# Kernel tuning notes

Measured on AMD Instinct MI355X. Metric: run time of the kernel, lower is better.

Reference implementation:

```python
import jax, jax.numpy as jnp
import numpy as np

N = 50000      # nodes
E = 800000     # edges (avg degree 16)
NFEAT = 256
NHID = 128
NCLASS = 40
NLAYERS_MID = 13  # gc2..gc14


def setup_inputs() -> dict:
    key = jax.random.key(0)
    ks = jax.random.split(key, 16)
    stdv_h = 1.0 / np.sqrt(NHID)     # GraphConvolution stdv = 1/sqrt(out_features)
    stdv_c = 1.0 / np.sqrt(NCLASS)
    u = lambda k, shape, s: jax.random.uniform(k, shape, jnp.float32, -s, s)
    return {
        "x": jax.random.normal(ks[0], (N, NFEAT), jnp.float32),
        "edge_src": jax.random.randint(ks[1], (E,), 0, N, jnp.int32),
        "edge_dst": jax.random.randint(ks[2], (E,), 0, N, jnp.int32),
        "edge_weight": jax.random.uniform(ks[3], (E,), jnp.float32),
        # skip-branch linear (self.weight / self.bias)
        "W0": u(ks[4], (NFEAT, NHID), stdv_h),
        "b0": u(ks[5], (NHID,), stdv_h),
        # gc1: nfeat -> nhid
        "W1": u(ks[6], (NFEAT, NHID), stdv_h),
        "b1": u(ks[7], (NHID,), stdv_h),
        # gc2..gc14: nhid -> nhid, stacked
        "Wmid": u(ks[8], (NLAYERS_MID, NHID, NHID), stdv_h),
        "bmid": u(ks[9], (NLAYERS_MID, NHID), stdv_h),
        # gc15: 14*nhid -> nclass
        "W15": u(ks[10], (14 * NHID, NCLASS), stdv_c),
        "b15": u(ks[11], (NCLASS,), stdv_c),
    }


def reference(x, edge_src, edge_dst, edge_weight, W0, b0, W1, b1, Wmid, bmid, W15, b15):
    n = x.shape[0]

    def gcn(h, W, b):
        # support = h @ W ; out = spmm(adj, support) + b  (adj as weighted edge list)
        support = h @ W
        msgs = support[edge_src] * edge_weight[:, None]           # [E, d]
        agg = jax.ops.segment_sum(msgs, edge_dst, num_segments=n)  # [N, d]
        return agg + b

    z = x @ W0 + b0
    x1 = jax.nn.relu(gcn(x, W1, b1)) + z

    def step(h, Wb):
        W, b = Wb
        hn = jax.nn.relu(gcn(h, W, b)) + h
        return hn, hn

    _, xs = jax.lax.scan(step, x1, (Wmid, bmid))   # xs: [13, N, NHID] = x2..x14
    all_x = jnp.concatenate([x1[None], xs], axis=0)  # [14, N, NHID] = x1..x14
    # concat order in torch code: (x14, x13, ..., x1)
    x_cat = jnp.swapaxes(all_x[::-1], 0, 1).reshape(n, 14 * NHID)
    # dropout is identity in eval mode
    x15 = gcn(x_cat, W15, b15)
    return jax.nn.log_softmax(x15, axis=1)
```

## Files before the change

### kernel.cpp

```cpp
#include <hip/hip_runtime.h>
#include <stdint.h>

#define NN 50000
#define EE 800000
#define DH 128
#define NC 40
#define KCAT (14*DH)
#define CAP 64

typedef __bf16 bf16x8 __attribute__((ext_vector_type(8)));
typedef float floatx4 __attribute__((ext_vector_type(4)));

#define GLOAD_LDS16(gp, lp)                                                          \
  __builtin_amdgcn_global_load_lds(                                                  \
      (const __attribute__((address_space(1))) uint32_t*)(gp),                       \
      (__attribute__((address_space(3))) uint32_t*)(lp), 16, 0, 0)

__device__ __forceinline__ float bf2f(unsigned short u) {
  union { uint32_t i; float f; } v; v.i = ((uint32_t)u) << 16; return v.f;
}
__device__ __forceinline__ unsigned short f2bf(float f) {
  union { float f; uint32_t i; } v; v.f = f;
  uint32_t x = v.i;
  uint32_t r = (x + 0x7fffu + ((x >> 16) & 1u)) >> 16;
  return (unsigned short)r;
}

__global__ void init_counts_detect(int* counts, const unsigned short* xw) {
  int i = blockIdx.x * blockDim.x + threadIdx.x;
  if (i < NN) counts[i] = 0;
  if (blockIdx.x == 0) {
    int t = threadIdx.x;
    int wild = 0;
    for (int k = t; k < 4096; k += 256) {
      unsigned e = (xw[k] >> 7) & 0xFF;
      if (e >= 0x90) wild++;
    }
    __shared__ int red[256];
    red[t] = wild;
    __syncthreads();
    for (int s = 128; s > 0; s >>= 1) {
      if (t < s) red[t] += red[t + s];
      __syncthreads();
    }
    if (t == 0) counts[NN] = red[0];
  }
}

__global__ void convert_f4(const void* in, unsigned short* outp, int n4, const int* flag) {
  bool isf32 = (*flag) > 32;
  for (int i = blockIdx.x * blockDim.x + threadIdx.x; i < n4;
       i += gridDim.x * blockDim.x) {
    ushort4 o;
    if (isf32) {
      float4 v = ((const float4*)in)[i];
      o.x = f2bf(v.x); o.y = f2bf(v.y); o.z = f2bf(v.z); o.w = f2bf(v.w);
    } else {
      o = ((const ushort4*)in)[i];
    }
    ((ushort4*)outp)[i] = o;
  }
}

__global__ void convert_bias(const void* b0, const void* b1, const void* bm,
                             const void* b15, unsigned short* bb, const int* flag) {
  bool isf32 = (*flag) > 32;
  int i = blockIdx.x * blockDim.x + threadIdx.x;
  if (i >= 1960) return;
  const void* src; int off;
  if (i < 128)        { src = b0;  off = i; }
  else if (i < 256)   { src = b1;  off = i - 128; }
  else if (i < 1920)  { src = bm;  off = i - 256; }
  else                { src = b15; off = i - 1920; }
  bb[i] = isf32 ? f2bf(((const float*)src)[off]) : ((const unsigned short*)src)[off];
}

__global__ void transpose_w(const void* B, unsigned short* BT,
                            int L, int K, int M, int Mpad, const int* flag) {
  bool isf32 = (*flag) > 32;
  int total = L * Mpad * K;
  for (int idx = blockIdx.x * blockDim.x + threadIdx.x; idx < total;
       idx += gridDim.x * blockDim.x) {
    int k = idx % K;
    int n = (idx / K) % Mpad;
    int l = idx / (K * Mpad);
    unsigned short v = 0;
    if (n < M) {
      size_t si = (size_t)l * K * M + (size_t)k * M + n;
      v = isf32 ? f2bf(((const float*)B)[si]) : ((const unsigned short*)B)[si];
    }
    BT[idx] = v;
  }
}

__global__ void build_ell(const int* __restrict__ src, const int* __restrict__ dst,
                          const void* __restrict__ w,
                          int* __restrict__ cnt, int2* __restrict__ ell,
                          const int* __restrict__ flag) {
  bool isf32 = (*flag) > 32;
  int e = blockIdx.x * blockDim.x + threadIdx.x;
  if (e >= EE) return;
  int d = dst[e];
  if ((unsigned)d >= NN) return;
  int p = atomicAdd(&cnt[d], 1);
  if (p >= CAP) return;
  int s = src[e];
  float wf = isf32 ? ((const float*)w)[e] : bf2f(((const unsigned short*)w)[e]);
  if ((unsigned)s >= NN) { s = 0; wf = 0.f; }
  union { float f; int i; } wv; wv.f = wf;
  ell[(size_t)d * CAP + p] = make_int2(s, wv.i);
}

__global__ void pad_ell(const int* __restrict__ cnt, int2* __restrict__ ell) {
  int wave = threadIdx.x >> 6, lane = threadIdx.x & 63;
  int row = blockIdx.x * 4 + wave;
  if (row >= NN) return;
  int n = cnt[row];
  if (n > CAP) n = CAP;
  int padn = (n + 7) & ~7;
  if (lane >= n && lane < padn) ell[(size_t)row * CAP + lane] = make_int2(0, 0);
}

__global__ __launch_bounds__(256) void gemm_first(
    const unsigned short* __restrict__ A,
    const unsigned short* __restrict__ BT,
    unsigned short* __restrict__ C0,
    unsigned short* __restrict__ C1,
    const unsigned short* __restrict__ bias) {
  __shared__ unsigned short As[64 * 256];
  int t = threadIdx.x;
  int wave = t >> 6, lane = t & 63;
  int q = lane >> 4, mn = lane & 15;
  int r0 = blockIdx.x * 64;

  #pragma unroll
  for (int cc = 0; cc < 8; ++cc) {
    int L = cc * 4096 + t * 16;
    int row = L >> 9;
    int colb = (L & 511) ^ ((row & 7) << 4);
    int gr = r0 + row; if (gr >= NN) gr = NN - 1;
    GLOAD_LDS16((const char*)A + (size_t)gr * 512 + colb, (char*)As + L);
  }
  __syncthreads();

  floatx4 acc[4][4];
  floatx4 zf = {0.f, 0.f, 0.f, 0.f};
  #pragma unroll
  for (int i = 0; i < 4; ++i)
    #pragma unroll
    for (int j = 0; j < 4; ++j) acc[i][j] = zf;

  #pragma unroll
  for (int ks = 0; ks < 8; ++ks) {
    bf16x8 fa[4], fb[4];
    #pragma unroll
    for (int i = 0; i < 4; ++i) {
      int row = i * 16 + mn;
      fa[i] = *(const bf16x8*)((const char*)As + row * 512 +
                               ((ks * 64 + q * 16) ^ ((row & 7) << 4)));
    }
    #pragma unroll
    for (int j = 0; j < 4; ++j)
      fb[j] = *(const bf16x8*)((const char*)BT +
                               (size_t)(wave * 64 + j * 16 + mn) * 512 + ks * 64 + q * 16);
    #pragma unroll
    for (int i = 0; i < 4; ++i)
      #pragma unroll
      for (int j = 0; j < 4; ++j)
        acc[i][j] = __builtin_amdgcn_mfma_f32_16x16x32_bf16(fa[i], fb[j], acc[i][j], 0, 0, 0);
  }

  #pragma unroll
  for (int j = 0; j < 4; ++j) {
    int col = wave * 64 + j * 16 + mn;
    bool is0 = col < 128;
    int ccol = is0 ? col : col - 128;
    unsigned short* Cp = is0 ? C0 : C1;
    float badd = is0 ? bf2f(bias[ccol]) : 0.f;
    #pragma unroll
    for (int i = 0; i < 4; ++i) {
      int rbase = r0 + i * 16 + q * 4;
      #pragma unroll
      for (int rr = 0; rr < 4; ++rr) {
        int row = rbase + rr;
        if (row < NN) Cp[(size_t)row * 128 + ccol] = f2bf(acc[i][j][rr] + badd);
      }
    }
  }
}

__global__ __launch_bounds__(256) void gemm_mid(
    const unsigned short* __restrict__ A,
    const unsigned short* __restrict__ BT,
    unsigned short* __restrict__ C) {
  __shared__ unsigned short As[32 * 128];
  int t = threadIdx.x;
  int wave = t >> 6, lane = t & 63;
  int q = lane >> 4, mn = lane & 15;
  int r0 = blockIdx.x * 32;

  #pragma unroll
  for (int cc = 0; cc < 2; ++cc) {
    int L = cc * 4096 + t * 16;
    int row = L >> 8;
    int colb = (L & 255) ^ ((row & 7) << 4);
    int gr = r0 + row; if (gr >= NN) gr = NN - 1;
    GLOAD_LDS16((const char*)A + (size_t)gr * (KCAT * 2) + colb, (char*)As + L);
  }
  __syncthreads();

  floatx4 acc[2][2];
  floatx4 zf = {0.f, 0.f, 0.f, 0.f};
  #pragma unroll
  for (int i = 0; i < 2; ++i)
    #pragma unroll
    for (int j = 0; j < 2; ++j) acc[i][j] = zf;

  #pragma unroll
  for (int ks = 0; ks < 4; ++ks) {
    bf16x8 fa[2], fb[2];
    #pragma unroll
    for (int i = 0; i < 2; ++i) {
      int row = i * 16 + mn;
      fa[i] = *(const bf16x8*)((const char*)As + row * 256 +
                               ((ks * 64 + q * 16) ^ ((row & 7) << 4)));
    }
    #pragma unroll
    for (int j = 0; j < 2; ++j)
      fb[j] = *(const bf16x8*)((const char*)BT +
                               (size_t)(wave * 32 + j * 16 + mn) * 256 + ks * 64 + q * 16);
    #pragma unroll
    for (int i = 0; i < 2; ++i)
      #pragma unroll
      for (int j = 0; j < 2; ++j)
        acc[i][j] = __builtin_amdgcn_mfma_f32_16x16x32_bf16(fa[i], fb[j], acc[i][j], 0, 0, 0);
  }

  #pragma unroll
  for (int i = 0; i < 2; ++i) {
    int rbase = r0 + i * 16 + q * 4;
    #pragma unroll
    for (int j = 0; j < 2; ++j) {
      int col = wave * 32 + j * 16 + mn;
      #pragma unroll
      for (int rr = 0; rr < 4; ++rr) {
        int row = rbase + rr;
        if (row < NN) C[(size_t)row * 128 + col] = f2bf(acc[i][j][rr]);
      }
    }
  }
}

__global__ __launch_bounds__(256) void gemm_cat3(
    const unsigned short* __restrict__ A,
    const unsigned short* __restrict__ BT,
    float* __restrict__ C) {
  __shared__ unsigned short As[2][64 * 128];
  int t = threadIdx.x;
  int wave = t >> 6, lane = t & 63;
  int q = lane >> 4, mn = lane & 15;
  int r0 = blockIdx.x * 64;

  floatx4 acc[3];
  floatx4 zf = {0.f, 0.f, 0.f, 0.f};
  #pragma unroll
  for (int j = 0; j < 3; ++j) acc[j] = zf;

  const char* bbase[3];
  #pragma unroll
  for (int j = 0; j < 3; ++j)
    bbase[j] = (const char*)BT + (size_t)(j * 16 + mn) * 3584 + q * 16;

  auto stage = [&](int c) {
    #pragma unroll
    for (int cc = 0; cc < 4; ++cc) {
      int L = cc * 4096 + t * 16;
      int row = L >> 8;
      int colb = (L & 255) ^ ((row & 7) << 4);
      int gr = r0 + row; if (gr >= NN) gr = NN - 1;
      GLOAD_LDS16((const char*)A + (size_t)gr * 3584 + c * 256 + colb,
                  (char*)As[c & 1] + L);
    }
  };

  stage(0);
  __syncthreads();
  int rloc = wave * 16 + mn;
  int rsw = (rloc & 7) << 4;
  for (int c = 0; c < 14; ++c) {
    bf16x8 fb[3][4];
    #pragma unroll
    for (int ks = 0; ks < 4; ++ks)
      #pragma unroll
      for (int j = 0; j < 3; ++j)
        fb[j][ks] = *(const bf16x8*)(bbase[j] + c * 256 + ks * 64);
    asm volatile("" ::: "memory");
    if (c + 1 < 14) stage(c + 1);
    asm volatile("" ::: "memory");
    const char* buf = (const char*)As[c & 1];
    #pragma unroll
    for (int ks = 0; ks < 4; ++ks) {
      bf16x8 fa = *(const bf16x8*)(buf + rloc * 256 + ((ks * 64 + q * 16) ^ rsw));
      #pragma unroll
      for (int j = 0; j < 3; ++j)
        acc[j] = __builtin_amdgcn_mfma_f32_16x16x32_bf16(fa, fb[j][ks], acc[j], 0, 0, 0);
    }
    if (c + 1 < 14) __syncthreads();
  }

  #pragma unroll
  for (int j = 0; j < 3; ++j) {
    int col = j * 16 + mn;
    if (col < NC) {
      #pragma unroll
      for (int rr = 0; rr < 4; ++rr) {
        int row = r0 + wave * 16 + q * 4 + rr;
        if (row < NN) C[(size_t)row * NC + col] = acc[j][rr];
      }
    }
  }
}

__global__ __launch_bounds__(256) void spmm_layer(
    const unsigned short* __restrict__ support, const int* __restrict__ cnt,
    const int2* __restrict__ ell, const unsigned short* __restrict__ bias,
    const unsigned short* __restrict__ res, int res_stride,
    unsigned short* __restrict__ out, int out_stride) {
  int wave = threadIdx.x >> 6, lane = threadIdx.x & 63;
  int row = blockIdx.x * 4 + wave;
  if (row >= NN) return;
  int n = cnt[row];
  if (n > CAP) n = CAP;
  int padn = (n + 7) & ~7;
  int2 ev = make_int2(0, 0);
  if (lane < padn) ev = ell[(size_t)row * CAP + lane];
  uint32_t bw = *(const uint32_t*)(bias + 2 * lane);
  uint32_t rw = *(const uint32_t*)(res + (size_t)row * res_stride + 2 * lane);

  float a0 = 0.f, a1 = 0.f;
  uint32_t gA[8], gB[8];
  auto load8 = [&](uint32_t* g, int j0) {
    #pragma unroll
    for (int u = 0; u < 8; ++u) {
      int s = __shfl(ev.x, j0 + u);
      g[u] = *(const uint32_t*)(support + (size_t)s * DH + 2 * lane);
    }
  };
  auto fma8 = [&](const uint32_t* g, int j0) {
    #pragma unroll
    for (int u = 0; u < 8; ++u) {
      union { int i; float f; } wv; wv.i = __shfl(ev.y, j0 + u);
      a0 += wv.f * bf2f((unsigned short)(g[u] & 0xffff));
      a1 += wv.f * bf2f((unsigned short)(g[u] >> 16));
    }
  };
  if (padn > 0) {
    load8(gA, 0);
    int b = 0;
    for (;;) {
      if (8 * (b + 1) < padn) load8(gB, 8 * (b + 1));
      fma8(gA, 8 * b);
      ++b; if (8 * b >= padn) break;
      if (8 * (b + 1) < padn) load8(gA, 8 * (b + 1));
      fma8(gB, 8 * b);
      ++b; if (8 * b >= padn) break;
    }
  }

  float v0 = fmaxf(a0 + bf2f((unsigned short)(bw & 0xffff)), 0.f) +
             bf2f((unsigned short)(rw & 0xffff));
  float v1 = fmaxf(a1 + bf2f((unsigned short)(bw >> 16)), 0.f) +
             bf2f((unsigned short)(rw >> 16));
  uint32_t o = (uint32_t)f2bf(v0) | ((uint32_t)f2bf(v1) << 16);
  *(uint32_t*)(out + (size_t)row * out_stride + 2 * lane) = o;
}

__global__ __launch_bounds__(256) void spmm_softmax_out(
    const float* __restrict__ s15, const int* __restrict__ cnt,
    const int2* __restrict__ ell, const unsigned short* __restrict__ bias,
    float* __restrict__ out) {
  int wave = threadIdx.x >> 6, lane = threadIdx.x & 63;
  int row = blockIdx.x * 4 + wave;
  if (row >= NN) return;
  int n = cnt[row];
  if (n > CAP) n = CAP;
  int padn = (n + 7) & ~7;
  int2 ev = make_int2(0, 0);
  if (lane < padn) ev = ell[(size_t)row * CAP + lane];
  int fl = lane < NC ? lane : NC - 1;
  float acc = 0.f;
  for (int j = 0; j < padn; j += 4) {
    float g[4];
    #pragma unroll
    for (int u = 0; u < 4; ++u) {
      int s = __shfl(ev.x, j + u);
      g[u] = s15[(size_t)s * NC + fl];
    }
    #pragma unroll
    for (int u = 0; u < 4; ++u) {
      union { int i; float f; } wv; wv.i = __shfl(ev.y, j + u);
      acc += wv.f * g[u];
    }
  }
  acc += bf2f(bias[fl]);
  float v = (lane < NC) ? acc : -3.0e38f;
  float m = v;
  #pragma unroll
  for (int off = 32; off > 0; off >>= 1) m = fmaxf(m, __shfl_xor(m, off));
  float e = (lane < NC) ? expf(v - m) : 0.f;
  float sum = e;
  #pragma unroll
  for (int off = 32; off > 0; off >>= 1) sum += __shfl_xor(sum, off);
  if (lane < NC) out[(size_t)row * NC + lane] = v - m - logf(sum);
}

extern "C" void kernel_launch(void* const* d_in, const int* in_sizes, int n_in,
                              void* d_out, int out_size, void* d_ws, size_t ws_size,
                              hipStream_t stream) {
  const void* x   = d_in[0];
  const int* esrc = (const int*)d_in[1];
  const int* edst = (const int*)d_in[2];
  const void* ew  = d_in[3];
  const void* W0  = d_in[4];
  const void* b0  = d_in[5];
  const void* W1  = d_in[6];
  const void* b1  = d_in[7];
  const void* Wm  = d_in[8];
  const void* bm  = d_in[9];
  const void* W15 = d_in[10];
  const void* b15 = d_in[11];
  float* out = (float*)d_out;

  char* ws = (char*)d_ws;
  size_t off = 0;
  auto alloc = [&](size_t bytes) -> void* {
    void* p = ws + off;
    off = (off + bytes + 255) & ~(size_t)255;
    return p;
  };
  unsigned short* xcat = (unsigned short*)alloc((size_t)NN * KCAT * 2);
  unsigned short* xbf  = (unsigned short*)alloc((size_t)NN * 256 * 2);
  unsigned short* supp = (unsigned short*)alloc((size_t)NN * DH * 2);
  unsigned short* zbuf = (unsigned short*)alloc((size_t)NN * DH * 2);
  float* s15           = (float*)alloc((size_t)NN * NC * 4);
  int* counts          = (int*)alloc((size_t)(NN + 1) * 4);
  int2* ell            = (int2*)alloc((size_t)NN * CAP * 8);
  unsigned short* W01T = (unsigned short*)alloc((size_t)256 * 256 * 2);
  unsigned short* WmT  = (unsigned short*)alloc((size_t)13 * 128 * 128 * 2);
  unsigned short* W15T = (unsigned short*)alloc((size_t)48 * 1792 * 2);
  unsigned short* bb   = (unsigned short*)alloc((size_t)(128 + 128 + 13 * 128 + 40) * 2);
  if (off > ws_size) return;
  int* flag = counts + NN;
  unsigned short* b0b  = bb;
  unsigned short* b1b  = bb + 128;
  unsigned short* bmb  = bb + 256;
  unsigned short* b15b = bb + 256 + 13 * 128;

  init_counts_detect<<<197, 256, 0, stream>>>(counts, (const unsigned short*)x);
  transpose_w<<<128, 256, 0, stream>>>(W0, W01T, 1, 256, 128, 128, flag);
  transpose_w<<<128, 256, 0, stream>>>(W1, W01T + 128 * 256, 1, 256, 128, 128, flag);
  transpose_w<<<832, 256, 0, stream>>>(Wm, WmT, 13, 128, 128, 128, flag);
  transpose_w<<<336, 256, 0, stream>>>(W15, W15T, 1, 1792, 40, 48, flag);
  convert_f4<<<2048, 256, 0, stream>>>(x, xbf, NN * 256 / 4, flag);
  convert_bias<<<8, 256, 0, stream>>>(b0, b1, bm, b15, bb, flag);
  build_ell<<<3125, 256, 0, stream>>>(esrc, edst, ew, counts, ell, flag);

  int gb64 = (NN + 63) / 64;
  int gb32 = (NN + 31) / 32;
  int sb   = (NN + 3) / 4;
  pad_ell<<<sb, 256, 0, stream>>>(counts, ell);
  gemm_first<<<gb64, 256, 0, stream>>>(xbf, W01T, zbuf, supp, b0b);
  spmm_layer<<<sb, 256, 0, stream>>>(supp, counts, ell, b1b, zbuf, DH,
                                     xcat + 13 * DH, KCAT);
  for (int l = 0; l < 13; ++l) {
    gemm_mid<<<gb32, 256, 0, stream>>>(xcat + (13 - l) * DH,
                                       WmT + l * 128 * 128, supp);
    spmm_layer<<<sb, 256, 0, stream>>>(supp, counts, ell, bmb + l * DH,
                                       xcat + (13 - l) * DH, KCAT,
                                       xcat + (12 - l) * DH, KCAT);
  }
  gemm_cat3<<<gb64, 256, 0, stream>>>(xcat, W15T, s15);
  spmm_softmax_out<<<sb, 256, 0, stream>>>(s15, counts, ell, b15b, out);
}
```

Before: 956.8 us.

## Slice SpMM rows across column quarters and deepen final GEMM pipeline

The SpMM layer kernel now splits each row's 128 features into four 64-byte column slices handled by separate blocks. Each wave processes four rows with 16 lanes each, so one 8-byte gather per lane becomes 16 lanes covering a contiguous 64-byte chunk. The aim is more parallelism and better memory-level concurrency for the gather-bound aggregation, at the cost of reading the ELL index data four times. The final concat GEMM moves from a 2-stage to a 4-stage LDS ring with explicit vmcnt waits and raw barriers, prefetching B fragments one step ahead, to overlap loads with MFMA work.

```diff
diff --git a/kernel.cpp b/kernel.cpp
--- a/kernel.cpp
+++ b/kernel.cpp
@@ -251,11 +251,11 @@
   }
 }
 
-__global__ __launch_bounds__(256) void gemm_cat3(
+__global__ __launch_bounds__(256) void gemm_cat4(
     const unsigned short* __restrict__ A,
     const unsigned short* __restrict__ BT,
     float* __restrict__ C) {
-  __shared__ unsigned short As[2][64 * 128];
+  __shared__ unsigned short As[4][64 * 128];
   int t = threadIdx.x;
   int wave = t >> 6, lane = t & 63;
   int q = lane >> 4, mn = lane & 15;
@@ -279,25 +279,34 @@
       int colb = (L & 255) ^ ((row & 7) << 4);
       int gr = r0 + row; if (gr >= NN) gr = NN - 1;
       GLOAD_LDS16((const char*)A + (size_t)gr * 3584 + c * 256 + colb,
-                  (char*)As[c & 1] + L);
+                  (char*)As[c & 3] + L);
     }
   };
 
+  bf16x8 fb[3][4];
+  auto loadB = [&](int c) {
+    #pragma unroll
+    for (int ks = 0; ks < 4; ++ks)
+      #pragma unroll
+      for (int j = 0; j < 3; ++j)
+        fb[j][ks] = *(const bf16x8*)(bbase[j] + c * 256 + ks * 64);
+  };
+
   stage(0);
-  __syncthreads();
+  asm volatile("" ::: "memory");
+  loadB(0);
+  asm volatile("" ::: "memory");
+  stage(1);
+  stage(2);
+
   int rloc = wave * 16 + mn;
   int rsw = (rloc & 7) << 4;
   for (int c = 0; c < 14; ++c) {
-    bf16x8 fb[3][4];
-    #pragma unroll
-    for (int ks = 0; ks < 4; ++ks)
-      #pragma unroll
-      for (int j = 0; j < 3; ++j)
-        fb[j][ks] = *(const bf16x8*)(bbase[j] + c * 256 + ks * 64);
-    asm volatile("" ::: "memory");
-    if (c + 1 < 14) stage(c + 1);
-    asm volatile("" ::: "memory");
-    const char* buf = (const char*)As[c & 1];
+    if (c == 0)      asm volatile("s_waitcnt vmcnt(8)" ::: "memory");
+    else if (c < 12) asm volatile("s_waitcnt vmcnt(4)" ::: "memory");
+    else             asm volatile("s_waitcnt vmcnt(0)" ::: "memory");
+    __builtin_amdgcn_s_barrier();
+    const char* buf = (const char*)As[c & 3];
     #pragma unroll
     for (int ks = 0; ks < 4; ++ks) {
       bf16x8 fa = *(const bf16x8*)(buf + rloc * 256 + ((ks * 64 + q * 16) ^ rsw));
@@ -305,7 +314,10 @@
       for (int j = 0; j < 3; ++j)
         acc[j] = __builtin_amdgcn_mfma_f32_16x16x32_bf16(fa, fb[j][ks], acc[j], 0, 0, 0);
     }
-    if (c + 1 < 14) __syncthreads();
+    asm volatile("" ::: "memory");
+    if (c + 1 < 14) loadB(c + 1);
+    asm volatile("" ::: "memory");
+    if (c + 3 < 14) stage(c + 3);
   }
 
   #pragma unroll
@@ -321,58 +333,72 @@
   }
 }
 
-__global__ __launch_bounds__(256) void spmm_layer(
+__global__ __launch_bounds__(256) void spmm_layer_sliced(
     const unsigned short* __restrict__ support, const int* __restrict__ cnt,
     const int2* __restrict__ ell, const unsigned short* __restrict__ bias,
     const unsigned short* __restrict__ res, int res_stride,
     unsigned short* __restrict__ out, int out_stride) {
+  int bid = blockIdx.x;
+  int slice = bid & 3;
+  int rblk = bid >> 2;
   int wave = threadIdx.x >> 6, lane = threadIdx.x & 63;
-  int row = blockIdx.x * 4 + wave;
-  if (row >= NN) return;
-  int n = cnt[row];
-  if (n > CAP) n = CAP;
+  int group = lane >> 4, gl = lane & 15;
+  int row = rblk * 16 + wave * 4 + group;
+  int colb = slice * 64 + gl * 4;
+
+  int n = cnt[row]; if (n > CAP) n = CAP;
   int padn = (n + 7) & ~7;
-  int2 ev = make_int2(0, 0);
-  if (lane < padn) ev = ell[(size_t)row * CAP + lane];
-  uint32_t bw = *(const uint32_t*)(bias + 2 * lane);
-  uint32_t rw = *(const uint32_t*)(res + (size_t)row * res_stride + 2 * lane);
-
+  const int2* erow = ell + (size_t)row * CAP;
+  int2 ev0 = (gl      < padn) ? erow[gl]      : make_int2(0, 0);
+  int2 ev1 = (gl + 16 < padn) ? erow[gl + 16] : make_int2(0, 0);
+  int2 ev2 = (gl + 32 < padn) ? erow[gl + 32] : make_int2(0, 0);
+  int2 ev3 = (gl + 48 < padn) ? erow[gl + 48] : make_int2(0, 0);
+
+  int wm = padn;
+  wm = max(wm, __shfl_xor(wm, 16));
+  wm = max(wm, __shfl_xor(wm, 32));
+
+  int srcbase = lane & 0x30;
   float a0 = 0.f, a1 = 0.f;
   uint32_t gA[8], gB[8];
-  auto load8 = [&](uint32_t* g, int j0) {
+
+  auto load8 = [&](uint32_t* g, int2 EV, int boff) {
     #pragma unroll
     for (int u = 0; u < 8; ++u) {
-      int s = __shfl(ev.x, j0 + u);
-      g[u] = *(const uint32_t*)(support + (size_t)s * DH + 2 * lane);
+      int s = __shfl(EV.x, srcbase + boff + u);
+      g[u] = *(const uint32_t*)((const char*)support + (size_t)s * 256 + colb);
     }
   };
-  auto fma8 = [&](const uint32_t* g, int j0) {
+  auto fma8 = [&](const uint32_t* g, int2 EV, int boff) {
     #pragma unroll
     for (int u = 0; u < 8; ++u) {
-      union { int i; float f; } wv; wv.i = __shfl(ev.y, j0 + u);
+      union { int i; float f; } wv; wv.i = __shfl(EV.y, srcbase + boff + u);
       a0 += wv.f * bf2f((unsigned short)(g[u] & 0xffff));
       a1 += wv.f * bf2f((unsigned short)(g[u] >> 16));
     }
   };
-  if (padn > 0) {
-    load8(gA, 0);
-    int b = 0;
-    for (;;) {
-      if (8 * (b + 1) < padn) load8(gB, 8 * (b + 1));
-      fma8(gA, 8 * b);
-      ++b; if (8 * b >= padn) break;
-      if (8 * (b + 1) < padn) load8(gA, 8 * (b + 1));
-      fma8(gB, 8 * b);
-      ++b; if (8 * b >= padn) break;
-    }
-  }
-
+
+  if (wm > 0) {
+    load8(gA, ev0, 0);
+    if (wm > 8)  load8(gB, ev0, 8);
+    fma8(gA, ev0, 0);
+    if (wm > 8)  { if (wm > 16) load8(gA, ev1, 0); fma8(gB, ev0, 8); }
+    if (wm > 16) { if (wm > 24) load8(gB, ev1, 8); fma8(gA, ev1, 0); }
+    if (wm > 24) { if (wm > 32) load8(gA, ev2, 0); fma8(gB, ev1, 8); }
+    if (wm > 32) { if (wm > 40) load8(gB, ev2, 8); fma8(gA, ev2, 0); }
+    if (wm > 40) { if (wm > 48) load8(gA, ev3, 0); fma8(gB, ev2, 8); }
+    if (wm > 48) { if (wm > 56) load8(gB, ev3, 8); fma8(gA, ev3, 0); }
+    if (wm > 56) fma8(gB, ev3, 8);
+  }
+
+  uint32_t bw = *(const uint32_t*)((const char*)bias + colb);
+  uint32_t rw = *(const uint32_t*)((const char*)res + (size_t)row * res_stride * 2 + colb);
   float v0 = fmaxf(a0 + bf2f((unsigned short)(bw & 0xffff)), 0.f) +
              bf2f((unsigned short)(rw & 0xffff));
   float v1 = fmaxf(a1 + bf2f((unsigned short)(bw >> 16)), 0.f) +
              bf2f((unsigned short)(rw >> 16));
   uint32_t o = (uint32_t)f2bf(v0) | ((uint32_t)f2bf(v1) << 16);
-  *(uint32_t*)(out + (size_t)row * out_stride + 2 * lane) = o;
+  *(uint32_t*)((char*)out + (size_t)row * out_stride * 2 + colb) = o;
 }
 
 __global__ __launch_bounds__(256) void spmm_softmax_out(
@@ -466,19 +492,20 @@
   build_ell<<<3125, 256, 0, stream>>>(esrc, edst, ew, counts, ell, flag);
 
   int gb64 = (NN + 63) / 64;
+  int sb   = (NN + 3) / 4;
   int gb32 = (NN + 31) / 32;
-  int sb   = (NN + 3) / 4;
+  int ssb  = (NN / 16) * 4;
   pad_ell<<<sb, 256, 0, stream>>>(counts, ell);
   gemm_first<<<gb64, 256, 0, stream>>>(xbf, W01T, zbuf, supp, b0b);
-  spmm_layer<<<sb, 256, 0, stream>>>(supp, counts, ell, b1b, zbuf, DH,
-                                     xcat + 13 * DH, KCAT);
+  spmm_layer_sliced<<<ssb, 256, 0, stream>>>(supp, counts, ell, b1b, zbuf, DH,
+                                             xcat + 13 * DH, KCAT);
   for (int l = 0; l < 13; ++l) {
     gemm_mid<<<gb32, 256, 0, stream>>>(xcat + (13 - l) * DH,
                                        WmT + l * 128 * 128, supp);
-    spmm_layer<<<sb, 256, 0, stream>>>(supp, counts, ell, bmb + l * DH,
-                                       xcat + (13 - l) * DH, KCAT,
-                                       xcat + (12 - l) * DH, KCAT);
-  }
-  gemm_cat3<<<gb64, 256, 0, stream>>>(xcat, W15T, s15);
+    spmm_layer_sliced<<<ssb, 256, 0, stream>>>(supp, counts, ell, bmb + l * DH,
+                                               xcat + (13 - l) * DH, KCAT,
+                                               xcat + (12 - l) * DH, KCAT);
+  }
+  gemm_cat4<<<gb64, 256, 0, stream>>>(xcat, W15T, s15);
   spmm_softmax_out<<<sb, 256, 0, stream>>>(s15, counts, ell, b15b, out);
 }
```

New measurement: 1.134 ms. +18.5%, slower.

## Sort rows by degree bucket and process four rows per wave in SpMM

Applied to the files above, without the earlier changes.

Adds a histogram, scan and scatter pass that builds a row permutation grouped by padded degree. The SpMM now gives each 16-lane group its own row and has each lane load 16-byte slices, so one wave handles four rows with similar trip counts. This aims to cut wasted lanes and divergence and to widen the gather loads. The final concat GEMM is also rewritten to a simpler 128-row tile that stages A and B in LDS with plain loads and no double buffering, which may lose overlap.

```diff
diff --git a/kernel.cpp b/kernel.cpp
--- a/kernel.cpp
+++ b/kernel.cpp
@@ -26,9 +26,10 @@
   return (unsigned short)r;
 }
 
-__global__ void init_counts_detect(int* counts, const unsigned short* xw) {
+__global__ void init_counts_detect(int* counts, int* hist, const unsigned short* xw) {
   int i = blockIdx.x * blockDim.x + threadIdx.x;
   if (i < NN) counts[i] = 0;
+  if (i < 16) hist[i] = 0;
   if (blockIdx.x == 0) {
     int t = threadIdx.x;
     int wild = 0;
@@ -121,6 +122,46 @@
   if (lane >= n && lane < padn) ell[(size_t)row * CAP + lane] = make_int2(0, 0);
 }
 
+__global__ void hist_padn(const int* __restrict__ cnt, int* __restrict__ hist) {
+  __shared__ int lh[9];
+  int t = threadIdx.x;
+  if (t < 9) lh[t] = 0;
+  __syncthreads();
+  int i = blockIdx.x * 256 + t;
+  if (i < NN) {
+    int n = cnt[i]; if (n > CAP) n = CAP;
+    atomicAdd(&lh[(n + 7) >> 3], 1);
+  }
+  __syncthreads();
+  if (t < 9 && lh[t]) atomicAdd(&hist[t], lh[t]);
+}
+
+__global__ void scan9(const int* __restrict__ hist, int* __restrict__ base) {
+  if (threadIdx.x == 0) {
+    int s = 0;
+    for (int k = 0; k < 9; ++k) { base[k] = s; s += hist[k]; }
+  }
+}
+
+__global__ void scatter_perm(const int* __restrict__ cnt, int* __restrict__ base,
+                             int* __restrict__ perm) {
+  __shared__ int lh[9], lbase[9];
+  int t = threadIdx.x;
+  if (t < 9) lh[t] = 0;
+  __syncthreads();
+  int i = blockIdx.x * 256 + t;
+  int b = 0, p = 0;
+  if (i < NN) {
+    int n = cnt[i]; if (n > CAP) n = CAP;
+    b = (n + 7) >> 3;
+    p = atomicAdd(&lh[b], 1);
+  }
+  __syncthreads();
+  if (t < 9) lbase[t] = lh[t] ? atomicAdd(&base[t], lh[t]) : 0;
+  __syncthreads();
+  if (i < NN) perm[lbase[b] + p] = i;
+}
+
 __global__ __launch_bounds__(256) void gemm_first(
     const unsigned short* __restrict__ A,
     const unsigned short* __restrict__ BT,
@@ -251,128 +292,153 @@
   }
 }
 
-__global__ __launch_bounds__(256) void gemm_cat3(
-    const unsigned short* __restrict__ A,
-    const unsigned short* __restrict__ BT,
+__global__ __launch_bounds__(256) void gemm_cat(
+    const unsigned short* __restrict__ A, const unsigned short* __restrict__ BT ,
     float* __restrict__ C) {
-  __shared__ unsigned short As[2][64 * 128];
+  __shared__ unsigned short As[128][40];
+  __shared__ unsigned short Bs[48][40];
   int t = threadIdx.x;
   int wave = t >> 6, lane = t & 63;
   int q = lane >> 4, mn = lane & 15;
-  int r0 = blockIdx.x * 64;
-
-  floatx4 acc[3];
+  int r0 = blockIdx.x * 128;
+  floatx4 acc[2][3];
   floatx4 zf = {0.f, 0.f, 0.f, 0.f};
   #pragma unroll
-  for (int j = 0; j < 3; ++j) acc[j] = zf;
-
-  const char* bbase[3];
-  #pragma unroll
-  for (int j = 0; j < 3; ++j)
-    bbase[j] = (const char*)BT + (size_t)(j * 16 + mn) * 3584 + q * 16;
-
-  auto stage = [&](int c) {
-    #pragma unroll
-    for (int cc = 0; cc < 4; ++cc) {
-      int L = cc * 4096 + t * 16;
-      int row = L >> 8;
-      int colb = (L & 255) ^ ((row & 7) << 4);
-      int gr = r0 + row; if (gr >= NN) gr = NN - 1;
-      GLOAD_LDS16((const char*)A + (size_t)gr * 3584 + c * 256 + colb,
-                  (char*)As[c & 1] + L);
-    }
-  };
-
-  stage(0);
-  __syncthreads();
-  int rloc = wave * 16 + mn;
-  int rsw = (rloc & 7) << 4;
-  for (int c = 0; c < 14; ++c) {
-    bf16x8 fb[3][4];
-    #pragma unroll
-    for (int ks = 0; ks < 4; ++ks)
+  for (int i = 0; i < 2; ++i)
+    #pragma unroll
+    for (int j = 0; j < 3; ++j) acc[i][j] = zf;
+
+  int arow = t >> 2;
+  int akc = (t & 3) << 3;
+
+  for (int k0 = 0; k0 < KCAT; k0 += 32) {
+    #pragma unroll
+    for (int h = 0; h < 2; ++h) {
+      int r = arow + h * 64;
+      uint4 v = make_uint4(0, 0, 0, 0);
+      if (r0 + r < NN) v = *(const uint4*)(A + (size_t)(r0 + r) * KCAT + k0 + akc);
+      *(uint4*)(&As[r][akc]) = v;
+    }
+    if (t < 192) {
+      uint4 v = *(const uint4*)(BT + (size_t)arow * KCAT + k0 + akc);
+      *(uint4*)(&Bs[arow][akc]) = v;
+    }
+    __syncthreads();
+    bf16x8 fa[2], fb[3];
+    #pragma unroll
+    for (int i = 0; i < 2; ++i) fa[i] = *(const bf16x8*)(&As[wave * 32 + i * 16 + mn][q * 8]);
+    #pragma unroll
+    for (int j = 0; j < 3; ++j) fb[j] = *(const bf16x8*)(&Bs[j * 16 + mn][q * 8]);
+    #pragma unroll
+    for (int i = 0; i < 2; ++i)
       #pragma unroll
       for (int j = 0; j < 3; ++j)
-        fb[j][ks] = *(const bf16x8*)(bbase[j] + c * 256 + ks * 64);
-    asm volatile("" ::: "memory");
-    if (c + 1 < 14) stage(c + 1);
-    asm volatile("" ::: "memory");
-    const char* buf = (const char*)As[c & 1];
-    #pragma unroll
-    for (int ks = 0; ks < 4; ++ks) {
-      bf16x8 fa = *(const bf16x8*)(buf + rloc * 256 + ((ks * 64 + q * 16) ^ rsw));
-      #pragma unroll
-      for (int j = 0; j < 3; ++j)
-        acc[j] = __builtin_amdgcn_mfma_f32_16x16x32_bf16(fa, fb[j][ks], acc[j], 0, 0, 0);
-    }
-    if (c + 1 < 14) __syncthreads();
-  }
-
-  #pragma unroll
-  for (int j = 0; j < 3; ++j) {
-    int col = j * 16 + mn;
-    if (col < NC) {
+        acc[i][j] = __builtin_amdgcn_mfma_f32_16x16x32_bf16(fa[i], fb[j], acc[i][j], 0, 0, 0);
+    __syncthreads();
+  }
+  #pragma unroll
+  for (int i = 0; i < 2; ++i) {
+    int rbase = r0 + wave * 32 + i * 16 + q * 4;
+    #pragma unroll
+    for (int j = 0; j < 3; ++j) {
+      int col = j * 16 + mn;
       #pragma unroll
       for (int rr = 0; rr < 4; ++rr) {
-        int row = r0 + wave * 16 + q * 4 + rr;
-        if (row < NN) C[(size_t)row * NC + col] = acc[j][rr];
+        int row = rbase + rr;
+        if (row < NN && col < NC) C[(size_t)row * NC + col] = acc[i][j][rr];
       }
     }
   }
 }
 
-__global__ __launch_bounds__(256) void spmm_layer(
+__global__ __launch_bounds__(256) void spmm_layer4(
     const unsigned short* __restrict__ support, const int* __restrict__ cnt,
-    const int2* __restrict__ ell, const unsigned short* __restrict__ bias,
+    const int2* __restrict__ ell, const int* __restrict__ perm,
+    const unsigned short* __restrict__ bias,
     const unsigned short* __restrict__ res, int res_stride,
     unsigned short* __restrict__ out, int out_stride) {
-  int wave = threadIdx.x >> 6, lane = threadIdx.x & 63;
-  int row = blockIdx.x * 4 + wave;
-  if (row >= NN) return;
-  int n = cnt[row];
-  if (n > CAP) n = CAP;
+  int t = threadIdx.x;
+  int wave = t >> 6, lane = t & 63;
+  int g = lane >> 4, gl = lane & 15;
+  int rix = blockIdx.x * 16 + wave * 4 + g;
+  int row = perm[rix];
+  int n = cnt[row]; if (n > CAP) n = CAP;
   int padn = (n + 7) & ~7;
-  int2 ev = make_int2(0, 0);
-  if (lane < padn) ev = ell[(size_t)row * CAP + lane];
-  uint32_t bw = *(const uint32_t*)(bias + 2 * lane);
-  uint32_t rw = *(const uint32_t*)(res + (size_t)row * res_stride + 2 * lane);
-
-  float a0 = 0.f, a1 = 0.f;
-  uint32_t gA[8], gB[8];
-  auto load8 = [&](uint32_t* g, int j0) {
-    #pragma unroll
-    for (int u = 0; u < 8; ++u) {
-      int s = __shfl(ev.x, j0 + u);
-      g[u] = *(const uint32_t*)(support + (size_t)s * DH + 2 * lane);
+  const int2* erow = ell + (size_t)row * CAP;
+  int2 ev0 = (gl      < padn) ? erow[gl]      : make_int2(0, 0);
+  int2 ev1 = (gl + 16 < padn) ? erow[gl + 16] : make_int2(0, 0);
+  int2 ev2 = (gl + 32 < padn) ? erow[gl + 32] : make_int2(0, 0);
+  int2 ev3 = (gl + 48 < padn) ? erow[gl + 48] : make_int2(0, 0);
+  int wmax = padn;
+  wmax = max(wmax, __shfl_xor(wmax, 16));
+  wmax = max(wmax, __shfl_xor(wmax, 32));
+  int srcbase = lane & 0x30;
+  int colb = gl * 16;
+
+  float a[8];
+  #pragma unroll
+  for (int e = 0; e < 8; ++e) a[e] = 0.f;
+  uint4 gA[4], gB[4];
+
+  auto load4 = [&](uint4* gbuf, int2 EV, int off) {
+    #pragma unroll
+    for (int u = 0; u < 4; ++u) {
+      int s = __shfl(EV.x, srcbase + off + u);
+      gbuf[u] = *(const uint4*)((const char*)support + (size_t)s * 256 + colb);
     }
   };
-  auto fma8 = [&](const uint32_t* g, int j0) {
-    #pragma unroll
-    for (int u = 0; u < 8; ++u) {
-      union { int i; float f; } wv; wv.i = __shfl(ev.y, j0 + u);
-      a0 += wv.f * bf2f((unsigned short)(g[u] & 0xffff));
-      a1 += wv.f * bf2f((unsigned short)(g[u] >> 16));
+  auto fma4 = [&](const uint4* gbuf, int2 EV, int off) {
+    #pragma unroll
+    for (int u = 0; u < 4; ++u) {
+      union { int i; float f; } wv; wv.i = __shfl(EV.y, srcbase + off + u);
+      uint32_t w[4] = {gbuf[u].x, gbuf[u].y, gbuf[u].z, gbuf[u].w};
+      #pragma unroll
+      for (int e = 0; e < 4; ++e) {
+        union { uint32_t i; float f; } lo, hi;
+        lo.i = w[e] << 16;
+        hi.i = w[e] & 0xffff0000u;
+        a[2 * e]     += wv.f * lo.f;
+        a[2 * e + 1] += wv.f * hi.f;
+      }
     }
   };
-  if (padn > 0) {
-    load8(gA, 0);
-    int b = 0;
-    for (;;) {
-      if (8 * (b + 1) < padn) load8(gB, 8 * (b + 1));
-      fma8(gA, 8 * b);
-      ++b; if (8 * b >= padn) break;
-      if (8 * (b + 1) < padn) load8(gA, 8 * (b + 1));
-      fma8(gB, 8 * b);
-      ++b; if (8 * b >= padn) break;
-    }
-  }
-
-  float v0 = fmaxf(a0 + bf2f((unsigned short)(bw & 0xffff)), 0.f) +
-             bf2f((unsigned short)(rw & 0xffff));
-  float v1 = fmaxf(a1 + bf2f((unsigned short)(bw >> 16)), 0.f) +
-             bf2f((unsigned short)(rw >> 16));
-  uint32_t o = (uint32_t)f2bf(v0) | ((uint32_t)f2bf(v1) << 16);
-  *(uint32_t*)(out + (size_t)row * out_stride + 2 * lane) = o;
+
+  if (wmax > 0) {
+    load4(gA, ev0, 0);
+                     load4(gB, ev0, 4);                    fma4(gA, ev0, 0);
+     { if (wmax >  8) load4(gA, ev0, 8);                   fma4(gB, ev0, 4); }
+    if (wmax >  8) { if (wmax > 12) load4(gB, ev0, 12);           fma4(gA, ev0, 8); }
+    if (wmax > 12) { if (wmax > 16) load4(gA, ev1, 0);            fma4(gB, ev0, 12); }
+    if (wmax > 16) { if (wmax > 20) load4(gB, ev1, 4);            fma4(gA, ev1, 0); }
+    if (wmax > 20) { if (wmax > 24) load4(gA, ev1, 8);            fma4(gB, ev1, 4); }
+    if (wmax > 24) { if (wmax > 28) load4(gB, ev1, 12);           fma4(gA, ev1, 8); }
+    if (wmax > 28) { if (wmax > 32) load4(gA, ev2, 0);            fma4(gB, ev1, 12); }
+    if (wmax > 32) { if (wmax > 36) load4(gB, ev2, 4);            fma4(gA, ev2, 0); }
+    if (wmax > 36) { if (wmax > 40) load4(gA, ev2, 8);            fma4(gB, ev2, 4); }
+    if (wmax > 40) { if (wmax > 44) load4(gB, ev2, 12);           fma4(gA, ev2, 8); }
+    if (wmax > 44) { if (wmax > 48) load4(gA, ev3, 0);            fma4(gB, ev2, 12); }
+    if (wmax > 48) { if (wmax > 52) load4(gB, ev3, 4);            fma4(gA, ev3, 0); }
+    if (wmax > 52) { if (wmax > 56) load4(gA, ev3, 8);            fma4(gB, ev3, 4); }
+    if (wmax > 56) { if (wmax > 60) load4(gB, ev3, 12);           fma4(gA, ev3, 8); }
+    if (wmax > 60) fma4(gB, ev3, 12);
+  }
+
+  uint4 bw = *(const uint4*)((const char*)bias + colb);
+  uint4 rw = *(const uint4*)((const char*)res + (size_t)row * res_stride * 2 + colb);
+  uint32_t bwa[4] = {bw.x, bw.y, bw.z, bw.w};
+  uint32_t rwa[4] = {rw.x, rw.y, rw.z, rw.w};
+  uint32_t ob[4];
+  #pragma unroll
+  for (int e = 0; e < 4; ++e) {
+    union { uint32_t i; float f; } blo, bhi, rlo, rhi;
+    blo.i = bwa[e] << 16; bhi.i = bwa[e] & 0xffff0000u;
+    rlo.i = rwa[e] << 16; rhi.i = rwa[e] & 0xffff0000u;
+    float v0 = fmaxf(a[2 * e] + blo.f, 0.f) + rlo.f;
+    float v1 = fmaxf(a[2 * e + 1] + bhi.f, 0.f) + rhi.f;
+    ob[e] = (uint32_t)f2bf(v0) | ((uint32_t)f2bf(v1) << 16);
+  }
+  uint4 ov = make_uint4(ob[0], ob[1], ob[2], ob[3]);
+  *(uint4*)((char*)out + (size_t)row * out_stride * 2 + colb) = ov;
 }
 
 __global__ __launch_bounds__(256) void spmm_softmax_out(
@@ -444,6 +510,9 @@
   unsigned short* zbuf = (unsigned short*)alloc((size_t)NN * DH * 2);
   float* s15           = (float*)alloc((size_t)NN * NC * 4);
   int* counts          = (int*)alloc((size_t)(NN + 1) * 4);
+  int* perm            = (int*)alloc((size_t)NN * 4);
+  int* hist            = (int*)alloc(64);
+  int* hbase           = (int*)alloc(64);
   int2* ell            = (int2*)alloc((size_t)NN * CAP * 8);
   unsigned short* W01T = (unsigned short*)alloc((size_t)256 * 256 * 2);
   unsigned short* WmT  = (unsigned short*)alloc((size_t)13 * 128 * 128 * 2);
@@ -456,7 +525,7 @@
   unsigned short* bmb  = bb + 256;
   unsigned short* b15b = bb + 256 + 13 * 128;
 
-  init_counts_detect<<<197, 256, 0, stream>>>(counts, (const unsigned short*)x);
+  init_counts_detect<<<197, 256, 0, stream>>>(counts, hist, (const unsigned short*)x);
   transpose_w<<<128, 256, 0, stream>>>(W0, W01T, 1, 256, 128, 128, flag);
   transpose_w<<<128, 256, 0, stream>>>(W1, W01T + 128 * 256, 1, 256, 128, 128, flag);
   transpose_w<<<832, 256, 0, stream>>>(Wm, WmT, 13, 128, 128, 128, flag);
@@ -465,20 +534,26 @@
   convert_bias<<<8, 256, 0, stream>>>(b0, b1, bm, b15, bb, flag);
   build_ell<<<3125, 256, 0, stream>>>(esrc, edst, ew, counts, ell, flag);
 
-  int gb64 = (NN + 63) / 64;
-  int gb32 = (NN + 31) / 32;
-  int sb   = (NN + 3) / 4;
+  int gb64  = (NN + 63) / 64;
+  int gb32  = (NN + 31) / 32;
+  int gb128 = (NN + 127) / 128;
+  int sb    = (NN + 3) / 4;
+  int pb    = (NN + 255) / 256;
+  int s4b   = NN / 16;
   pad_ell<<<sb, 256, 0, stream>>>(counts, ell);
+  hist_padn<<<pb, 256, 0, stream>>>(counts, hist);
+  scan9<<<1, 64, 0, stream>>>(hist, hbase);
+  scatter_perm<<<pb, 256, 0, stream>>>(counts, hbase, perm);
   gemm_first<<<gb64, 256, 0, stream>>>(xbf, W01T, zbuf, supp, b0b);
-  spmm_layer<<<sb, 256, 0, stream>>>(supp, counts, ell, b1b, zbuf, DH,
-                                     xcat + 13 * DH, KCAT);
+  spmm_layer4<<<s4b, 256, 0, stream>>>(supp, counts, ell, perm, b1b, zbuf, DH,
+                                       xcat + 13 * DH, KCAT);
   for (int l = 0; l < 13; ++l) {
     gemm_mid<<<gb32, 256, 0, stream>>>(xcat + (13 - l) * DH,
                                        WmT + l * 128 * 128, supp);
-    spmm_layer<<<sb, 256, 0, stream>>>(supp, counts, ell, bmb + l * DH,
-                                       xcat + (13 - l) * DH, KCAT,
-                                       xcat + (12 - l) * DH, KCAT);
-  }
-  gemm_cat3<<<gb64, 256, 0, stream>>>(xcat, W15T, s15);
+    spmm_layer4<<<s4b, 256, 0, stream>>>(supp, counts, ell, perm, bmb + l * DH,
+                                         xcat + (13 - l) * DH, KCAT,
+                                         xcat + (12 - l) * DH, KCAT);
+  }
+  gemm_cat<<<gb128, 256, 0, stream>>>(xcat, W15T, s15);
   spmm_softmax_out<<<sb, 256, 0, stream>>>(s15, counts, ell, b15b, out);
 }
```

After: 949.5 us. No clear change (-0.8%).
